# Performance work log

Hardware: AMD Instinct MI355X
Metric: run time of the kernel (lower is better)

## Reference

```python
import jax, jax.numpy as jnp
import numpy as np

B, L_TEXT, N_TOKEN = 8, 2048, 2048
C_TEXT, C_OUT = 3584, 384
C_HID = C_OUT * 2
CHAIN_TYPES = (1, 2)   # heavy, light
CDR_TYPES = (2, 4, 6)  # CDR1/2/3


def setup_inputs() -> dict:
    key = jax.random.key(0)
    ks = jax.random.split(key, 10)
    text_conditioning = jax.random.normal(ks[0], (B, L_TEXT, C_TEXT), jnp.float32)
    text_mask = jnp.ones((B, L_TEXT), jnp.int32)
    chain_type_ids = jax.random.randint(ks[1], (B, L_TEXT), 0, 3).astype(jnp.int32)
    cdr_region_type_ids = jax.random.randint(ks[2], (B, L_TEXT), 0, 10).astype(jnp.int32)
    boltz_chain_type = jax.random.randint(ks[3], (B, N_TOKEN), 0, 4).astype(jnp.int32)
    boltz_region_type = jax.random.randint(ks[4], (B, N_TOKEN), 0, 10).astype(jnp.int32)
    W1 = jax.random.normal(ks[5], (C_HID, C_TEXT), jnp.float32) * 0.02
    b1 = jnp.zeros((C_HID,), jnp.float32)
    W2 = jax.random.normal(ks[6], (C_OUT, C_HID), jnp.float32) * 0.02
    b2 = jnp.zeros((C_OUT,), jnp.float32)
    scale = jnp.ones((1,), jnp.float32)
    return {
        "text_conditioning": text_conditioning, "text_mask": text_mask,
        "chain_type_ids": chain_type_ids, "cdr_region_type_ids": cdr_region_type_ids,
        "boltz_chain_type": boltz_chain_type, "boltz_region_type": boltz_region_type,
        "W1": W1, "b1": b1, "W2": W2, "b2": b2, "scale": scale,
    }


def _align_one(text_proj, tmask, pmask):
    # text_proj: [L, C]; tmask: [L] bool (text CDR positions); pmask: [N] bool (protein CDR positions)
    # The k-th masked text token (in sequence order) maps to the k-th masked protein token,
    # for k < min(n_text, n_protein). Other protein positions get zeros.
    L = tmask.shape[0]
    trank = jnp.cumsum(tmask) - 1          # rank among text CDR tokens
    n_text = jnp.sum(tmask)
    prank = jnp.cumsum(pmask) - 1          # rank among protein CDR tokens
    # idx_by_rank[r] = text index whose rank is r; out-of-range scatter indices dropped
    idx_by_rank = jnp.zeros((L,), jnp.int32).at[jnp.where(tmask, trank, L)].set(
        jnp.arange(L, dtype=jnp.int32), mode="drop")
    valid = pmask & (prank < n_text)       # prank < n_protein holds by construction under pmask
    src = idx_by_rank[jnp.clip(prank, 0, L - 1)]
    emb = text_proj[src]                   # [N, C]
    return jnp.where(valid[:, None], emb, jnp.zeros((), text_proj.dtype))


def reference(text_conditioning, text_mask, chain_type_ids, cdr_region_type_ids,
              boltz_chain_type, boltz_region_type, W1, b1, W2, b2, scale):
    # 2-layer MLP projection: c_text -> 2*c_out -> c_out with SiLU
    h = jax.nn.silu(jnp.einsum("blt,ht->blh", text_conditioning, W1) + b1)
    text_proj = jnp.einsum("blh,ch->blc", h, W2) + b2    # [B, L, C_OUT]

    tm = text_mask.astype(bool)
    result = jnp.zeros((text_conditioning.shape[0], boltz_chain_type.shape[1], W2.shape[0]),
                       text_proj.dtype)
    align = jax.vmap(_align_one)
    for ct in CHAIN_TYPES:
        for rt in CDR_TYPES:
            tmask = (chain_type_ids == ct) & (cdr_region_type_ids == rt) & tm
            pmask = (boltz_chain_type == ct) & (boltz_region_type == rt)
            # (chain, cdr) pairs write to disjoint protein positions, so add is exact
            result = result + align(text_proj, tmask, pmask)
    return scale * result
```

## Files before the change

### kernel.cpp

```cpp
#include <hip/hip_runtime.h>
#include <hip/hip_bf16.h>
#include <math.h>

typedef __bf16 bf16_t;
typedef bf16_t bf16x8 __attribute__((ext_vector_type(8)));
typedef bf16_t bf16x4 __attribute__((ext_vector_type(4)));
typedef float f32x4 __attribute__((ext_vector_type(4)));

#define L_TEXT 2048
#define N_TOKEN 2048
#define C_TEXT 3584
#define C_OUT 384
#define C_HID 768
#define BATCH 8
#define MAXROWS (BATCH * N_TOKEN)
#define PM 3072
#define KSPLIT 4
#define KCHUNK (C_TEXT / KSPLIT)
#define KSPLIT2 2
#define KCHUNK2 (C_HID / KSPLIT2)

#define NW1 (C_HID * C_TEXT / 8)
#define NW2 (C_OUT * C_HID / 8)
#define NINV (MAXROWS / 4)
#define NINIT (NW1 + NW2 + NINV + 1)
#define GCH (C_TEXT / 8)

__global__ __launch_bounds__(256) void init_cvt_kernel(
    const float* __restrict__ W1, const float* __restrict__ W2,
    bf16_t* __restrict__ W1b, bf16_t* __restrict__ W2b,
    int* __restrict__ inv, int* __restrict__ count) {
    int idx = blockIdx.x * 256 + threadIdx.x;
    if (idx < NW1) {
        int i = idx * 8;
        float4 v0 = *(const float4*)(W1 + i);
        float4 v1 = *(const float4*)(W1 + i + 4);
        bf16x8 o;
        o[0] = (bf16_t)v0.x; o[1] = (bf16_t)v0.y; o[2] = (bf16_t)v0.z; o[3] = (bf16_t)v0.w;
        o[4] = (bf16_t)v1.x; o[5] = (bf16_t)v1.y; o[6] = (bf16_t)v1.z; o[7] = (bf16_t)v1.w;
        *(bf16x8*)(W1b + i) = o;
    } else if (idx < NW1 + NW2) {
        int i = (idx - NW1) * 8;
        float4 v0 = *(const float4*)(W2 + i);
        float4 v1 = *(const float4*)(W2 + i + 4);
        bf16x8 o;
        o[0] = (bf16_t)v0.x; o[1] = (bf16_t)v0.y; o[2] = (bf16_t)v0.z; o[3] = (bf16_t)v0.w;
        o[4] = (bf16_t)v1.x; o[5] = (bf16_t)v1.y; o[6] = (bf16_t)v1.z; o[7] = (bf16_t)v1.w;
        *(bf16x8*)(W2b + i) = o;
    } else if (idx < NW1 + NW2 + NINV) {
        int i = idx - NW1 - NW2;
        int4 m1 = {-1, -1, -1, -1};
        ((int4*)inv)[i] = m1;
    } else if (idx == NW1 + NW2 + NINV) {
        *count = 0;
    }
}

__global__ __launch_bounds__(64) void map_kernel(
    const int* __restrict__ tm, const int* __restrict__ ctid,
    const int* __restrict__ cdrid, const int* __restrict__ bct,
    const int* __restrict__ brt,
    int* __restrict__ rows_src, int* __restrict__ inv,
    int* __restrict__ count) {
    __shared__ int trow[L_TEXT];
    const int bp = blockIdx.x;
    const int b = bp / 6, p = bp % 6;
    const int ct = (p < 3) ? 1 : 2;
    const int rt = 2 + 2 * (p % 3);
    const int lane = threadIdx.x;
    const unsigned long long ltm = (1ull << lane) - 1ull;

    unsigned int tbits = 0, pbits = 0;
#pragma unroll
    for (int i = 0; i < 32; i++) {
        int l = i * 64 + lane;
        unsigned int m = (ctid[b * L_TEXT + l] == ct) &&
                         (cdrid[b * L_TEXT + l] == rt) &&
                         (tm[b * L_TEXT + l] != 0);
        tbits |= m << i;
    }
#pragma unroll
    for (int i = 0; i < 32; i++) {
        int n = i * 64 + lane;
        unsigned int m = (bct[b * N_TOKEN + n] == ct) &&
                         (brt[b * N_TOKEN + n] == rt);
        pbits |= m << i;
    }

    int base = 0;
#pragma unroll
    for (int i = 0; i < 32; i++) {
        bool m = (tbits >> i) & 1;
        unsigned long long bal = __ballot(m);
        if (m) trow[base + __popcll(bal & ltm)] = i * 64 + lane;
        base += __popcll(bal);
    }
    const int n_text = base;
    __syncthreads();

    base = 0;
#pragma unroll
    for (int i = 0; i < 32; i++) {
        bool m = (pbits >> i) & 1;
        unsigned long long bal = __ballot(m);
        if (m) {
            int pr = base + __popcll(bal & ltm);
            if (pr < n_text) {
                int idx = atomicAdd(count, 1);
                if (idx < PM) {
                    rows_src[idx] = b * L_TEXT + trow[pr];
                    inv[b * N_TOKEN + i * 64 + lane] = idx;
                }
            }
        }
        base += __popcll(bal);
    }
}

__global__ __launch_bounds__(256) void gather_kernel(
    const float* __restrict__ X, const int* __restrict__ rows_src,
    const int* __restrict__ countp, bf16_t* __restrict__ Xg) {
    int count = *countp; if (count > PM) count = PM;
    int idx = blockIdx.x * 256 + threadIdx.x;
    int m = idx / GCH;
    if (m >= count) return;
    int c = (idx % GCH) * 8;
    const float* src = X + (size_t)rows_src[m] * C_TEXT + c;
    float4 v0 = *(const float4*)(src);
    float4 v1 = *(const float4*)(src + 4);
    bf16x8 o;
    o[0] = (bf16_t)v0.x; o[1] = (bf16_t)v0.y; o[2] = (bf16_t)v0.z; o[3] = (bf16_t)v0.w;
    o[4] = (bf16_t)v1.x; o[5] = (bf16_t)v1.y; o[6] = (bf16_t)v1.z; o[7] = (bf16_t)v1.w;
    *(bf16x8*)(Xg + (size_t)m * C_TEXT + c) = o;
}

__global__ __launch_bounds__(256) void gemm1_kernel(
    const bf16_t* __restrict__ Xg, const bf16_t* __restrict__ W1b,
    const int* __restrict__ countp, float* __restrict__ P) {
    int count = *countp; if (count > PM) count = PM;
    const int m0 = blockIdx.x * 128;
    if (m0 >= count) return;
    const int n0 = blockIdx.y * 128;
    const int kbeg = blockIdx.z * KCHUNK;

    __shared__ __align__(16) bf16_t As[2][128][40];
    __shared__ __align__(16) bf16_t Bs[2][128][40];

    const int t = threadIdx.x;
    const int lane = t & 63;
    const int w = t >> 6;
    const int wr = w >> 1, wc = w & 1;
    const int fr = lane & 15;
    const int kq = (lane >> 4) * 8;

    f32x4 acc[4][4];
#pragma unroll
    for (int i = 0; i < 4; i++)
#pragma unroll
        for (int j = 0; j < 4; j++) acc[i][j] = (f32x4){0.f, 0.f, 0.f, 0.f};

    const bf16_t* ap[2];
    const bf16_t* bp[2];
    int ofs[2];
#pragma unroll
    for (int j = 0; j < 2; j++) {
        int c = t + 256 * j;
        int row = c >> 2, c8 = (c & 3) * 8;
        ap[j] = Xg + (size_t)(m0 + row) * C_TEXT + kbeg + c8;
        bp[j] = W1b + (size_t)(n0 + row) * C_TEXT + kbeg + c8;
        ofs[j] = row * 40 + c8;
    }

    bf16_t* AsF = &As[0][0][0];
    bf16_t* BsF = &Bs[0][0][0];
    const int BUF = 128 * 40;

    bf16x8 ra[2], rb[2];
#pragma unroll
    for (int j = 0; j < 2; j++) { ra[j] = *(const bf16x8*)(ap[j]); rb[j] = *(const bf16x8*)(bp[j]); }

    const int T = KCHUNK / 32;
    for (int tile = 0; tile < T; ++tile) {
        const int cur = tile & 1;
#pragma unroll
        for (int j = 0; j < 2; j++) {
            *(bf16x8*)(AsF + cur * BUF + ofs[j]) = ra[j];
            *(bf16x8*)(BsF + cur * BUF + ofs[j]) = rb[j];
        }
        bf16x8 na[2], nb[2];
        bool more = (tile + 1 < T);
        if (more) {
            int k = (tile + 1) * 32;
#pragma unroll
            for (int j = 0; j < 2; j++) {
                na[j] = *(const bf16x8*)(ap[j] + k);
                nb[j] = *(const bf16x8*)(bp[j] + k);
            }
        }
        __syncthreads();
        bf16x8 af[4], bfr[4];
#pragma unroll
        for (int mi = 0; mi < 4; mi++)
            af[mi] = *(const bf16x8*)(AsF + cur * BUF + (wr * 64 + mi * 16 + fr) * 40 + kq);
#pragma unroll
        for (int ni = 0; ni < 4; ni++)
            bfr[ni] = *(const bf16x8*)(BsF + cur * BUF + (wc * 64 + ni * 16 + fr) * 40 + kq);
#pragma unroll
        for (int mi = 0; mi < 4; mi++)
#pragma unroll
            for (int ni = 0; ni < 4; ni++)
                acc[mi][ni] = __builtin_amdgcn_mfma_f32_16x16x32_bf16(
                    af[mi], bfr[ni], acc[mi][ni], 0, 0, 0);
        if (more) {
#pragma unroll
            for (int j = 0; j < 2; j++) { ra[j] = na[j]; rb[j] = nb[j]; }
        }
    }

    float* Pk = P + (size_t)blockIdx.z * PM * C_HID;
    const int rj = (lane >> 4) * 4;
#pragma unroll
    for (int mi = 0; mi < 4; mi++) {
#pragma unroll
        for (int ni = 0; ni < 4; ni++) {
            int gn = n0 + wc * 64 + ni * 16 + fr;
#pragma unroll
            for (int j = 0; j < 4; j++) {
                int gm = m0 + wr * 64 + mi * 16 + rj + j;
                if (gm < count) Pk[(size_t)gm * C_HID + gn] = acc[mi][ni][j];
            }
        }
    }
}

__global__ __launch_bounds__(256) void reduce1_kernel(
    const float* __restrict__ P, const float* __restrict__ b1,
    const int* __restrict__ countp, bf16_t* __restrict__ H) {
    int count = *countp; if (count > PM) count = PM;
    int idx = blockIdx.x * 256 + threadIdx.x;
    int m = idx / (C_HID / 4);
    int c = (idx % (C_HID / 4)) * 4;
    if (m >= count) return;
    f32x4 s = *(const f32x4*)(P + (size_t)m * C_HID + c);
#pragma unroll
    for (int ks = 1; ks < KSPLIT; ks++)
        s += *(const f32x4*)(P + ((size_t)ks * PM + m) * C_HID + c);
    f32x4 bb = *(const f32x4*)(b1 + c);
    bf16x4 o;
#pragma unroll
    for (int j = 0; j < 4; j++) {
        float v = s[j] + bb[j];
        o[j] = (bf16_t)(v / (1.0f + __expf(-v)));
    }
    *(bf16x4*)(H + (size_t)m * C_HID + c) = o;
}

__global__ __launch_bounds__(256) void gemm2_kernel(
    const bf16_t* __restrict__ Hm, const bf16_t* __restrict__ W2b,
    const int* __restrict__ countp, float* __restrict__ P2) {
    int count = *countp; if (count > PM) count = PM;
    const int m0 = blockIdx.x * 64;
    if (m0 >= count) return;
    const int n0 = blockIdx.y * 128;
    const int kbeg = blockIdx.z * KCHUNK2;

    __shared__ __align__(16) bf16_t As[2][64][40];
    __shared__ __align__(16) bf16_t Bs[2][128][40];

    const int t = threadIdx.x;
    const int lane = t & 63;
    const int w = t >> 6;
    const int wr = w >> 1, wc = w & 1;
    const int fr = lane & 15;
    const int kq = (lane >> 4) * 8;

    f32x4 acc[2][4];
#pragma unroll
    for (int i = 0; i < 2; i++)
#pragma unroll
        for (int j = 0; j < 4; j++) acc[i][j] = (f32x4){0.f, 0.f, 0.f, 0.f};

    const int arow = t >> 2, ac8 = (t & 3) * 8;
    const bf16_t* ap = Hm + (size_t)(m0 + arow) * C_HID + kbeg + ac8;
    const int aofs = arow * 40 + ac8;
    const bf16_t* bp[2];
    int bofs[2];
#pragma unroll
    for (int j = 0; j < 2; j++) {
        int c = t + 256 * j;
        int row = c >> 2, c8 = (c & 3) * 8;
        bp[j] = W2b + (size_t)(n0 + row) * C_HID + kbeg + c8;
        bofs[j] = row * 40 + c8;
    }

    bf16_t* AsF = &As[0][0][0];
    bf16_t* BsF = &Bs[0][0][0];
    const int ABUF = 64 * 40, BBUF = 128 * 40;

    bf16x8 ra = *(const bf16x8*)(ap);
    bf16x8 rb0 = *(const bf16x8*)(bp[0]);
    bf16x8 rb1 = *(const bf16x8*)(bp[1]);

    const int T = KCHUNK2 / 32;
    for (int tile = 0; tile < T; ++tile) {
        const int cur = tile & 1;
        *(bf16x8*)(AsF + cur * ABUF + aofs) = ra;
        *(bf16x8*)(BsF + cur * BBUF + bofs[0]) = rb0;
        *(bf16x8*)(BsF + cur * BBUF + bofs[1]) = rb1;
        bf16x8 na, nb0, nb1;
        bool more = (tile + 1 < T);
        if (more) {
            int k = (tile + 1) * 32;
            na = *(const bf16x8*)(ap + k);
            nb0 = *(const bf16x8*)(bp[0] + k);
            nb1 = *(const bf16x8*)(bp[1] + k);
        }
        __syncthreads();
        bf16x8 af[2], bfr[4];
#pragma unroll
        for (int mi = 0; mi < 2; mi++)
            af[mi] = *(const bf16x8*)(AsF + cur * ABUF + (wr * 32 + mi * 16 + fr) * 40 + kq);
#pragma unroll
        for (int ni = 0; ni < 4; ni++)
            bfr[ni] = *(const bf16x8*)(BsF + cur * BBUF + (wc * 64 + ni * 16 + fr) * 40 + kq);
#pragma unroll
        for (int mi = 0; mi < 2; mi++)
#pragma unroll
            for (int ni = 0; ni < 4; ni++)
                acc[mi][ni] = __builtin_amdgcn_mfma_f32_16x16x32_bf16(
                    af[mi], bfr[ni], acc[mi][ni], 0, 0, 0);
        if (more) { ra = na; rb0 = nb0; rb1 = nb1; }
    }

    float* Pk = P2 + (size_t)blockIdx.z * PM * C_OUT;
    const int rj = (lane >> 4) * 4;
#pragma unroll
    for (int mi = 0; mi < 2; mi++) {
#pragma unroll
        for (int ni = 0; ni < 4; ni++) {
            int gn = n0 + wc * 64 + ni * 16 + fr;
#pragma unroll
            for (int j = 0; j < 4; j++) {
                int gm = m0 + wr * 32 + mi * 16 + rj + j;
                if (gm < count) Pk[(size_t)gm * C_OUT + gn] = acc[mi][ni][j];
            }
        }
    }
}

__global__ __launch_bounds__(256) void out_kernel(
    const float* __restrict__ P2, const float* __restrict__ b2,
    const int* __restrict__ inv, const float* __restrict__ scale,
    float* __restrict__ out) {
    int idx = blockIdx.x * 256 + threadIdx.x;
    int token = idx / (C_OUT / 4);
    int c = (idx % (C_OUT / 4)) * 4;
    int m = inv[token];
    f32x4 o = (f32x4){0.f, 0.f, 0.f, 0.f};
    if (m >= 0) {
        f32x4 s = *(const f32x4*)(P2 + (size_t)m * C_OUT + c);
#pragma unroll
        for (int ks = 1; ks < KSPLIT2; ks++)
            s += *(const f32x4*)(P2 + ((size_t)ks * PM + m) * C_OUT + c);
        f32x4 bb = *(const f32x4*)(b2 + c);
        const float sc = scale[0];
#pragma unroll
        for (int j = 0; j < 4; j++) o[j] = sc * (s[j] + bb[j]);
    }
    *(f32x4*)(out + (size_t)token * C_OUT + c) = o;
}

extern "C" void kernel_launch(void* const* d_in, const int* in_sizes, int n_in,
                              void* d_out, int out_size, void* d_ws, size_t ws_size,
                              hipStream_t stream) {
    const float* X     = (const float*)d_in[0];
    const int*   tm    = (const int*)d_in[1];
    const int*   ctid  = (const int*)d_in[2];
    const int*   cdrid = (const int*)d_in[3];
    const int*   bct   = (const int*)d_in[4];
    const int*   brt   = (const int*)d_in[5];
    const float* W1    = (const float*)d_in[6];
    const float* b1    = (const float*)d_in[7];
    const float* W2    = (const float*)d_in[8];
    const float* b2    = (const float*)d_in[9];
    const float* scale = (const float*)d_in[10];

    char* ws = (char*)d_ws;
    size_t off = 0;
    int* count = (int*)(ws + off);        off += 1024;
    int* rows_src = (int*)(ws + off);     off += (size_t)PM * 4;
    int* inv = (int*)(ws + off);          off += (size_t)MAXROWS * 4;
    bf16_t* W1b = (bf16_t*)(ws + off);    off += (size_t)C_HID * C_TEXT * 2;
    bf16_t* W2b = (bf16_t*)(ws + off);    off += (size_t)C_OUT * C_HID * 2;
    bf16_t* Xg = (bf16_t*)(ws + off);     off += (size_t)PM * C_TEXT * 2;
    bf16_t* H = (bf16_t*)(ws + off);      off += (size_t)PM * C_HID * 2;
    float* P = (float*)(ws + off);        off += (size_t)KSPLIT * PM * C_HID * 4;
    float* P2 = P;

    init_cvt_kernel<<<(NINIT + 255) / 256, 256, 0, stream>>>(W1, W2, W1b, W2b,
                                                             inv, count);

    map_kernel<<<BATCH * 6, 64, 0, stream>>>(tm, ctid, cdrid, bct, brt,
                                             rows_src, inv, count);

    gather_kernel<<<(PM * GCH) / 256, 256, 0, stream>>>(X, rows_src, count, Xg);

    dim3 g1(PM / 128, C_HID / 128, KSPLIT);
    gemm1_kernel<<<g1, 256, 0, stream>>>(Xg, W1b, count, P);

    reduce1_kernel<<<(PM * C_HID / 4) / 256, 256, 0, stream>>>(P, b1, count, H);

    dim3 g2(PM / 64, C_OUT / 128, KSPLIT2);
    gemm2_kernel<<<g2, 256, 0, stream>>>(H, W2b, count, P2);

    out_kernel<<<(MAXROWS * C_OUT / 4) / 256, 256, 0, stream>>>(
        P2, b2, inv, scale, (float*)d_out);
}
```

Baseline: 136.1 us.

## Fuse mask ranking into the weight-convert kernel and write compacted rows deterministically

Moves the per-(batch,chain,CDR) mask ranking into extra blocks of the weight-conversion kernel, so it runs concurrently with the bf16 casts and one dependent launch is hidden. A new light kernel computes prefix offsets from per-pair valid counts and writes rows_src/inv without a global atomic. This makes the row ordering deterministic and removes atomic contention. It adds workspace lists and an extra global-memory round trip for the rank lists.

```diff
diff --git a/kernel.cpp b/kernel.cpp
--- a/kernel.cpp
+++ b/kernel.cpp
@@ -15,6 +15,7 @@
 #define BATCH 8
 #define MAXROWS (BATCH * N_TOKEN)
 #define PM 3072
+#define NPAIR (BATCH * 6)
 #define KSPLIT 4
 #define KCHUNK (C_TEXT / KSPLIT)
 #define KSPLIT2 2
@@ -23,13 +24,66 @@
 #define NW1 (C_HID * C_TEXT / 8)
 #define NW2 (C_OUT * C_HID / 8)
 #define NINV (MAXROWS / 4)
-#define NINIT (NW1 + NW2 + NINV + 1)
+#define CVT_BLOCKS ((NW1 + NW2 + NINV) / 256)
 #define GCH (C_TEXT / 8)
 
-__global__ __launch_bounds__(256) void init_cvt_kernel(
+__global__ __launch_bounds__(256) void init_map_kernel(
     const float* __restrict__ W1, const float* __restrict__ W2,
     bf16_t* __restrict__ W1b, bf16_t* __restrict__ W2b,
-    int* __restrict__ inv, int* __restrict__ count) {
+    int* __restrict__ inv,
+    const int* __restrict__ tm, const int* __restrict__ ctid,
+    const int* __restrict__ cdrid, const int* __restrict__ bct,
+    const int* __restrict__ brt,
+    int* __restrict__ trowL, int* __restrict__ pidxL, int* __restrict__ vcnt) {
+    if (blockIdx.x >= CVT_BLOCKS) {
+        const int bp = blockIdx.x - CVT_BLOCKS;
+        const int lane = threadIdx.x;
+        if (lane >= 64) return;
+        const int b = bp / 6, p = bp % 6;
+        const int ct = (p < 3) ? 1 : 2;
+        const int rt = 2 + 2 * (p % 3);
+        const unsigned long long ltm = (1ull << lane) - 1ull;
+
+        unsigned int tbits = 0, pbits = 0;
+#pragma unroll
+        for (int i = 0; i < 32; i++) {
+            int l = i * 64 + lane;
+            unsigned int m = (ctid[b * L_TEXT + l] == ct) &&
+                             (cdrid[b * L_TEXT + l] == rt) &&
+                             (tm[b * L_TEXT + l] != 0);
+            tbits |= m << i;
+        }
+#pragma unroll
+        for (int i = 0; i < 32; i++) {
+            int n = i * 64 + lane;
+            unsigned int m = (bct[b * N_TOKEN + n] == ct) &&
+                             (brt[b * N_TOKEN + n] == rt);
+            pbits |= m << i;
+        }
+
+        int base = 0;
+#pragma unroll
+        for (int i = 0; i < 32; i++) {
+            bool m = (tbits >> i) & 1;
+            unsigned long long bal = __ballot(m);
+            if (m) trowL[bp * L_TEXT + base + __popcll(bal & ltm)] = i * 64 + lane;
+            base += __popcll(bal);
+        }
+        const int n_text = base;
+
+        base = 0;
+#pragma unroll
+        for (int i = 0; i < 32; i++) {
+            bool m = (pbits >> i) & 1;
+            unsigned long long bal = __ballot(m);
+            if (m) pidxL[bp * L_TEXT + base + __popcll(bal & ltm)] = i * 64 + lane;
+            base += __popcll(bal);
+        }
+        const int n_prot = base;
+        if (lane == 0) vcnt[bp] = n_text < n_prot ? n_text : n_prot;
+        return;
+    }
+
     int idx = blockIdx.x * 256 + threadIdx.x;
     if (idx < NW1) {
         int i = idx * 8;
@@ -47,73 +101,34 @@
         o[0] = (bf16_t)v0.x; o[1] = (bf16_t)v0.y; o[2] = (bf16_t)v0.z; o[3] = (bf16_t)v0.w;
         o[4] = (bf16_t)v1.x; o[5] = (bf16_t)v1.y; o[6] = (bf16_t)v1.z; o[7] = (bf16_t)v1.w;
         *(bf16x8*)(W2b + i) = o;
-    } else if (idx < NW1 + NW2 + NINV) {
+    } else {
         int i = idx - NW1 - NW2;
         int4 m1 = {-1, -1, -1, -1};
         ((int4*)inv)[i] = m1;
-    } else if (idx == NW1 + NW2 + NINV) {
-        *count = 0;
-    }
-}
-
-__global__ __launch_bounds__(64) void map_kernel(
-    const int* __restrict__ tm, const int* __restrict__ ctid,
-    const int* __restrict__ cdrid, const int* __restrict__ bct,
-    const int* __restrict__ brt,
-    int* __restrict__ rows_src, int* __restrict__ inv,
-    int* __restrict__ count) {
-    __shared__ int trow[L_TEXT];
+    }
+}
+
+__global__ __launch_bounds__(64) void map_write_kernel(
+    const int* __restrict__ trowL, const int* __restrict__ pidxL,
+    const int* __restrict__ vcnt,
+    int* __restrict__ rows_src, int* __restrict__ inv, int* __restrict__ count) {
     const int bp = blockIdx.x;
-    const int b = bp / 6, p = bp % 6;
-    const int ct = (p < 3) ? 1 : 2;
-    const int rt = 2 + 2 * (p % 3);
+    const int b = bp / 6;
     const int lane = threadIdx.x;
-    const unsigned long long ltm = (1ull << lane) - 1ull;
-
-    unsigned int tbits = 0, pbits = 0;
-#pragma unroll
-    for (int i = 0; i < 32; i++) {
-        int l = i * 64 + lane;
-        unsigned int m = (ctid[b * L_TEXT + l] == ct) &&
-                         (cdrid[b * L_TEXT + l] == rt) &&
-                         (tm[b * L_TEXT + l] != 0);
-        tbits |= m << i;
-    }
-#pragma unroll
-    for (int i = 0; i < 32; i++) {
-        int n = i * 64 + lane;
-        unsigned int m = (bct[b * N_TOKEN + n] == ct) &&
-                         (brt[b * N_TOKEN + n] == rt);
-        pbits |= m << i;
-    }
-
-    int base = 0;
-#pragma unroll
-    for (int i = 0; i < 32; i++) {
-        bool m = (tbits >> i) & 1;
-        unsigned long long bal = __ballot(m);
-        if (m) trow[base + __popcll(bal & ltm)] = i * 64 + lane;
-        base += __popcll(bal);
-    }
-    const int n_text = base;
-    __syncthreads();
-
-    base = 0;
-#pragma unroll
-    for (int i = 0; i < 32; i++) {
-        bool m = (pbits >> i) & 1;
-        unsigned long long bal = __ballot(m);
-        if (m) {
-            int pr = base + __popcll(bal & ltm);
-            if (pr < n_text) {
-                int idx = atomicAdd(count, 1);
-                if (idx < PM) {
-                    rows_src[idx] = b * L_TEXT + trow[pr];
-                    inv[b * N_TOKEN + i * 64 + lane] = idx;
-                }
-            }
-        }
-        base += __popcll(bal);
+    int base = 0, total = 0;
+    for (int q = 0; q < NPAIR; q++) {
+        int v = vcnt[q];
+        if (q < bp) base += v;
+        total += v;
+    }
+    if (bp == 0 && lane == 0) *count = total < PM ? total : PM;
+    const int v = vcnt[bp];
+    for (int r = lane; r < v; r += 64) {
+        int g = base + r;
+        if (g < PM) {
+            rows_src[g] = b * L_TEXT + trowL[bp * L_TEXT + r];
+            inv[b * N_TOKEN + pidxL[bp * L_TEXT + r]] = g;
+        }
     }
 }
 
@@ -388,8 +403,11 @@
     char* ws = (char*)d_ws;
     size_t off = 0;
     int* count = (int*)(ws + off);        off += 1024;
+    int* vcnt = (int*)(ws + off);         off += 1024;
     int* rows_src = (int*)(ws + off);     off += (size_t)PM * 4;
     int* inv = (int*)(ws + off);          off += (size_t)MAXROWS * 4;
+    int* trowL = (int*)(ws + off);        off += (size_t)NPAIR * L_TEXT * 4;
+    int* pidxL = (int*)(ws + off);        off += (size_t)NPAIR * L_TEXT * 4;
     bf16_t* W1b = (bf16_t*)(ws + off);    off += (size_t)C_HID * C_TEXT * 2;
     bf16_t* W2b = (bf16_t*)(ws + off);    off += (size_t)C_OUT * C_HID * 2;
     bf16_t* Xg = (bf16_t*)(ws + off);     off += (size_t)PM * C_TEXT * 2;
@@ -397,11 +415,11 @@
     float* P = (float*)(ws + off);        off += (size_t)KSPLIT * PM * C_HID * 4;
     float* P2 = P;
 
-    init_cvt_kernel<<<(NINIT + 255) / 256, 256, 0, stream>>>(W1, W2, W1b, W2b,
-                                                             inv, count);
-
-    map_kernel<<<BATCH * 6, 64, 0, stream>>>(tm, ctid, cdrid, bct, brt,
-                                             rows_src, inv, count);
+    init_map_kernel<<<CVT_BLOCKS + NPAIR, 256, 0, stream>>>(
+        W1, W2, W1b, W2b, inv, tm, ctid, cdrid, bct, brt, trowL, pidxL, vcnt);
+
+    map_write_kernel<<<NPAIR, 64, 0, stream>>>(trowL, pidxL, vcnt,
+                                               rows_src, inv, count);
 
     gather_kernel<<<(PM * GCH) / 256, 256, 0, stream>>>(X, rows_src, count, Xg);
 
```

Result: faster. 126.5 us (-7.1%).
